# Kernel tuning notes

Hardware: AMD Instinct MI355X
Metric: run time of the kernel (lower is better)

Reference implementation:

```python
import jax, jax.numpy as jnp
import numpy as np

B, N, C = 8, 4096, 512
H = 8
OUT = 512
DH = C // H  # 64
LN_EPS = 1e-5
L2_EPS = 1e-12


def setup_inputs() -> dict:
    key = jax.random.key(0)
    ks = jax.random.split(key, 6)
    x = jax.random.normal(ks[0], (B, N, C), dtype=jnp.float32)
    ln_g = jnp.ones((C,), dtype=jnp.float32)
    ln_b = jnp.zeros((C,), dtype=jnp.float32)
    qkv_w = jax.random.normal(ks[1], (3 * C, C), dtype=jnp.float32) * 0.02  # torch Linear weight [out,in]
    temperature = jnp.ones((H, 1, 1), dtype=jnp.float32)
    proj_w = jax.random.normal(ks[2], (OUT, C), dtype=jnp.float32) * 0.02
    proj_b = jnp.zeros((OUT,), dtype=jnp.float32)
    return {"x": x, "ln_g": ln_g, "ln_b": ln_b, "qkv_w": qkv_w,
            "temperature": temperature, "proj_w": proj_w, "proj_b": proj_b}


def reference(x, ln_g, ln_b, qkv_w, temperature, proj_w, proj_b):
    # LayerNorm
    mu = jnp.mean(x, axis=-1, keepdims=True)
    var = jnp.mean(jnp.square(x - mu), axis=-1, keepdims=True)
    xn = (x - mu) * jax.lax.rsqrt(var + LN_EPS) * ln_g + ln_b
    # QKV projection (no bias)
    qkv = xn @ qkv_w.T  # [B,N,3C]
    qkv = qkv.reshape(B, N, 3, H, DH).transpose(2, 0, 3, 4, 1)  # [3,B,H,DH,N]
    q, k, v = qkv[0], qkv[1], qkv[2]  # each [B,H,DH,N] (already 'transposed' channel layout)
    # L2-normalize q,k along token dim (matches F.normalize eps behavior)
    q = q / jnp.clip(jnp.linalg.norm(q, axis=-1, keepdims=True), L2_EPS)
    k = k / jnp.clip(jnp.linalg.norm(k, axis=-1, keepdims=True), L2_EPS)
    # channel attention [B,H,DH,DH], scaled by per-head temperature
    attn = jnp.einsum('bhdn,bhen->bhde', q, k) * temperature[None]
    attn = jax.nn.softmax(attn, axis=-1)
    out = jnp.einsum('bhde,bhen->bhdn', attn, v)  # [B,H,DH,N]
    out = out.transpose(0, 3, 1, 2).reshape(B, N, H * DH)  # [B,N,C]
    out = jax.nn.gelu(out, approximate=False)
    out = out @ proj_w.T + proj_b
    return out
```

## Files before the change

kernel.cpp:

```cpp
#include <hip/hip_runtime.h>
#include <hip/hip_bf16.h>

typedef __hip_bfloat16 bf16;
typedef __bf16 bfrag __attribute__((ext_vector_type(8)));
typedef float f32x4 __attribute__((ext_vector_type(4)));

#define AS1 __attribute__((address_space(1)))
#define AS3 __attribute__((address_space(3)))

static constexpr int Bb = 8, Nn = 4096, Cc = 512, Hh = 8;
static constexpr int Mtok = Bb * Nn;
static constexpr int QKVC = 3 * Cc;
static constexpr size_t WS_NEED = 57147392;
static constexpr int SPL_STRIDE = 8 * 20 * 8192;

__device__ __forceinline__ void gl_lds16(const void* g, void* l) {
  __builtin_amdgcn_global_load_lds((const AS1 void*)g, (AS3 void*)l, 16, 0, 0);
}
__device__ __forceinline__ float gelu_exact(float x) {
  return 0.5f * x * (1.0f + erff(x * 0.70710678118654752f));
}
__device__ __forceinline__ int g3(int x) { return ((x & 1) << 2) | (x >> 1); }
__device__ __forceinline__ int tileid(int mt, int nt) {
  return mt + (nt == 0 ? 0 : nt == 1 ? 2 : nt == 2 ? 6 : 12);
}

__global__ __launch_bounds__(256) void fill_f32(float* o, float val, int n) {
  int i = blockIdx.x * 256 + threadIdx.x;
  if (i < n) o[i] = val;
}

__global__ __launch_bounds__(256) void cvt_f32_bf16(const float* __restrict__ a,
                                                    bf16* __restrict__ o, int n) {
  int i = (blockIdx.x * 256 + threadIdx.x) * 8;
  if (i + 8 <= n) {
    float f[8];
    *(float4*)f       = *(const float4*)(a + i);
    *(float4*)(f + 4) = *(const float4*)(a + i + 4);
    bf16 v[8];
#pragma unroll
    for (int j = 0; j < 8; ++j) v[j] = __float2bfloat16(f[j]);
    *(uint4*)(o + i) = *(uint4*)v;
  }
}

__global__ __launch_bounds__(256) void cvt_mirror(const float* __restrict__ part,
                                                  bf16* __restrict__ Gcvb) {
  int tile = blockIdx.x, b = blockIdx.y;
  int ti = tile >> 2, tj = tile & 3;
  int t = threadIdx.x;
  bf16* ob = Gcvb + (size_t)b * Cc * Cc;
  if (ti <= tj) {
#pragma unroll
    for (int r8 = 0; r8 < 8; ++r8) {
      int row = r8 * 16 + (t >> 4), col = (t & 15) * 8;
      int mt = 2 * ti + (row >> 6), rsub = row & 63;
      const float* p0 = part + ((size_t)b * 20 + tileid(mt, tj)) * 8192 + rsub * 128 + col;
      float f[8];
      *(float4*)f       = *(const float4*)p0;
      *(float4*)(f + 4) = *(const float4*)(p0 + 4);
#pragma unroll
      for (int s = 1; s < 4; ++s) {
        const float* ps = p0 + (size_t)s * SPL_STRIDE;
        float g[8];
        *(float4*)g       = *(const float4*)ps;
        *(float4*)(g + 4) = *(const float4*)(ps + 4);
#pragma unroll
        for (int j = 0; j < 8; ++j) f[j] += g[j];
      }
      bf16 v[8];
#pragma unroll
      for (int j = 0; j < 8; ++j) v[j] = __float2bfloat16(f[j]);
      *(uint4*)(ob + (size_t)(ti * 128 + row) * Cc + tj * 128 + col) = *(uint4*)v;
    }
  } else {
    __shared__ bf16 ls[128][136];
#pragma unroll
    for (int r8 = 0; r8 < 8; ++r8) {
      int srow = r8 * 16 + (t >> 4), scol = (t & 15) * 8;
      int mt = 2 * tj + (srow >> 6), rsub = srow & 63;
      const float* p0 = part + ((size_t)b * 20 + tileid(mt, ti)) * 8192 + rsub * 128 + scol;
      float f[8];
      *(float4*)f       = *(const float4*)p0;
      *(float4*)(f + 4) = *(const float4*)(p0 + 4);
#pragma unroll
      for (int s = 1; s < 4; ++s) {
        const float* ps = p0 + (size_t)s * SPL_STRIDE;
        float g[8];
        *(float4*)g       = *(const float4*)ps;
        *(float4*)(g + 4) = *(const float4*)(ps + 4);
#pragma unroll
        for (int j = 0; j < 8; ++j) f[j] += g[j];
      }
      bf16 v[8];
#pragma unroll
      for (int j = 0; j < 8; ++j) v[j] = __float2bfloat16(f[j]);
      *(uint4*)&ls[srow][scol] = *(uint4*)v;
    }
    __syncthreads();
#pragma unroll
    for (int r8 = 0; r8 < 8; ++r8) {
      int orow = r8 * 16 + (t >> 4), ocol = (t & 15) * 8;
      bf16 v[8];
#pragma unroll
      for (int u = 0; u < 8; ++u) v[u] = ls[ocol + u][orow];
      *(uint4*)(ob + (size_t)(ti * 128 + orow) * Cc + tj * 128 + ocol) = *(uint4*)v;
    }
  }
}

__global__ __launch_bounds__(256) void ln_kernel(const float* __restrict__ x,
                                                 const float* __restrict__ gw,
                                                 const float* __restrict__ bw,
                                                 bf16* __restrict__ xn) {
  int tok  = blockIdx.x * 4 + (threadIdx.x >> 6);
  int lane = threadIdx.x & 63;
  const float* xr = x + (size_t)tok * Cc + lane * 8;
  float f[8];
  *(float4*)f       = *(const float4*)xr;
  *(float4*)(f + 4) = *(const float4*)(xr + 4);
  float s = 0.f;
#pragma unroll
  for (int j = 0; j < 8; ++j) s += f[j];
#pragma unroll
  for (int m = 32; m; m >>= 1) s += __shfl_xor(s, m);
  float mu = s * (1.0f / 512.0f);
  float q = 0.f;
#pragma unroll
  for (int j = 0; j < 8; ++j) { float d = f[j] - mu; q += d * d; }
#pragma unroll
  for (int m = 32; m; m >>= 1) q += __shfl_xor(q, m);
  float rstd = rsqrtf(q * (1.0f / 512.0f) + 1e-5f);
  bf16 o[8];
#pragma unroll
  for (int j = 0; j < 8; ++j)
    o[j] = __float2bfloat16((f[j] - mu) * rstd * gw[lane * 8 + j] + bw[lane * 8 + j]);
  *(uint4*)(xn + (size_t)tok * Cc + lane * 8) = *(uint4*)o;
}

template <typename TC, bool SWZ>
__global__ __launch_bounds__(256) void gemm_bt(const bf16* __restrict__ A,
                                               const bf16* __restrict__ B,
                                               TC* __restrict__ C,
                                               int M, int N, int K,
                                               const float* __restrict__ bias,
                                               long sA_z, long sB_z, long sC_z) {
  A += (size_t)blockIdx.z * sA_z;
  B += (size_t)blockIdx.z * sB_z;
  C += (size_t)blockIdx.z * sC_z;
  __shared__ __align__(16) bf16 smem[16384];
  bf16* sA = smem;
  bf16* sB = smem + 8192;
  int t = threadIdx.x, w = t >> 6, lane = t & 63, fr = lane & 15, quad = lane >> 4;
  int n0, m0;
  if constexpr (SWZ) {
    int flat = blockIdx.y * 4 + blockIdx.x;
    int idx  = (flat & 7) * 128 + (flat >> 3);
    n0 = (idx & 3) * 128;
    m0 = (idx >> 2) * 128;
  } else {
    n0 = blockIdx.x * 128;
    m0 = blockIdx.y * 128;
  }
  int wm = (w >> 1) * 64, wn = (w & 1) * 64;
  f32x4 acc[4][4] = {};

  for (int k0 = 0; k0 < K; k0 += 64) {
    __syncthreads();
#pragma unroll
    for (int c2 = 0; c2 < 4; ++c2) {
      int c = w * 4 + c2;
      int row = c * 8 + (lane >> 3);
      int ke  = ((lane & 7) ^ (lane >> 3)) * 8;
      gl_lds16(A + (size_t)(m0 + row) * K + k0 + ke, (char*)sA + c * 1024);
      gl_lds16(B + (size_t)(n0 + row) * K + k0 + ke, (char*)sB + c * 1024);
    }
    __syncthreads();
#pragma unroll
    for (int kk = 0; kk < 64; kk += 32) {
      bfrag af[4], bg[4];
#pragma unroll
      for (int i = 0; i < 4; ++i)
        af[i] = *(const bfrag*)(sA + (wm + i * 16 + fr) * 64 +
                                ((((kk >> 3) + quad) ^ (fr & 7)) * 8));
#pragma unroll
      for (int j = 0; j < 4; ++j)
        bg[j] = *(const bfrag*)(sB + (wn + j * 16 + fr) * 64 +
                                ((((kk >> 3) + quad) ^ (fr & 7)) * 8));
#pragma unroll
      for (int i = 0; i < 4; ++i)
#pragma unroll
        for (int j = 0; j < 4; ++j)
          acc[i][j] = __builtin_amdgcn_mfma_f32_16x16x32_bf16(af[i], bg[j], acc[i][j], 0, 0, 0);
    }
  }

  if constexpr (__is_same(TC, float)) {
#pragma unroll
    for (int j = 0; j < 4; ++j) {
      float bj = bias ? bias[n0 + wn + j * 16 + fr] : 0.0f;
#pragma unroll
      for (int i = 0; i < 4; ++i)
#pragma unroll
        for (int r = 0; r < 4; ++r)
          C[(size_t)(m0 + wm + i * 16 + quad * 4 + r) * N + n0 + wn + j * 16 + fr] =
              acc[i][j][r] + bj;
    }
  } else {
    __syncthreads();
    bf16* ct = smem;
#pragma unroll
    for (int j = 0; j < 4; ++j) {
      float bj = bias ? bias[n0 + wn + j * 16 + fr] : 0.0f;
#pragma unroll
      for (int i = 0; i < 4; ++i)
#pragma unroll
        for (int r = 0; r < 4; ++r)
          ct[(wm + i * 16 + quad * 4 + r) * 128 + wn + j * 16 + fr] =
              __float2bfloat16(acc[i][j][r] + bj);
    }
    __syncthreads();
#pragma unroll
    for (int r8 = 0; r8 < 8; ++r8) {
      int row = r8 * 16 + (t >> 4);
      int ce  = (t & 15) * 8;
      *(uint4*)(C + (size_t)(m0 + row) * N + n0 + ce) = *(const uint4*)(smem + row * 128 + ce);
    }
  }
}

__global__ __launch_bounds__(256) void xtx(const bf16* __restrict__ xn,
                                           float* __restrict__ part) {
  int flat = blockIdx.x;
  int idx  = (flat & 7) * 80 + (flat >> 3);
  int tile = idx % 20;
  int sb   = idx / 20;
  int split = sb & 3, b = sb >> 2;
  int nt = tile < 2 ? 0 : tile < 6 ? 1 : tile < 12 ? 2 : 3;
  int mt = tile - (nt == 0 ? 0 : nt == 1 ? 2 : nt == 2 ? 6 : 12);
  int m0 = mt * 64, n0 = nt * 128;
  bool alias = ((mt >> 1) == nt);
  int t = threadIdx.x, w = t >> 6, lane = t & 63, fr = lane & 15, quad = lane >> 4;
  int wn = w * 32;
  __shared__ __align__(16) bf16 sB[8192];
  __shared__ __align__(16) bf16 sAb[4096];
  bf16* sA = alias ? (sB + (mt & 1) * 4096) : sAb;
  f32x4 acc[4][2] = {};
  const bf16* xb = xn + ((size_t)b * Nn + split * 1024) * Cc;
  int ch0b = (t & 15) * 8, tgb = t >> 4;
  int ch0a = (t & 7) * 8,  tga = t >> 3;
  bool doA = (!alias) && (t < 128);
  unsigned swz = (unsigned)g3(t & 7);
  unsigned wposb = (((unsigned)(tgb >> 1) ^ swz) * 16u) + (unsigned)(tgb & 1) * 8u;
  unsigned wposa = (((unsigned)(tga >> 1) ^ swz) * 16u) + (unsigned)(tga & 1) * 8u;
  uint4 va[4], vb[4];
#pragma unroll
  for (int j = 0; j < 4; ++j)
    vb[j] = *(const uint4*)(xb + (size_t)(tgb * 4 + j) * Cc + n0 + ch0b);
  if (doA)
#pragma unroll
    for (int j = 0; j < 4; ++j)
      va[j] = *(const uint4*)(xb + (size_t)(tga * 4 + j) * Cc + m0 + ch0a);
  for (int kc = 0; kc < 16; ++kc) {
    __syncthreads();
#pragma unroll
    for (int k = 0; k < 4; ++k) {
      unsigned b0 = ((const unsigned*)&vb[0])[k], b1 = ((const unsigned*)&vb[1])[k];
      unsigned b2 = ((const unsigned*)&vb[2])[k], b3 = ((const unsigned*)&vb[3])[k];
      uint2 lo = { (b0 & 0xffffu) | (b1 << 16), (b2 & 0xffffu) | (b3 << 16) };
      uint2 hi = { (b0 >> 16) | (b1 & 0xffff0000u), (b2 >> 16) | (b3 & 0xffff0000u) };
      *(uint2*)((char*)sB + (unsigned)(ch0b + 2 * k) * 128 + wposb) = lo;
      *(uint2*)((char*)sB + (unsigned)(ch0b + 2 * k + 1) * 128 + wposb) = hi;
    }
    if (doA) {
#pragma unroll
      for (int k = 0; k < 4; ++k) {
        unsigned a0 = ((const unsigned*)&va[0])[k], a1 = ((const unsigned*)&va[1])[k];
        unsigned a2 = ((const unsigned*)&va[2])[k], a3 = ((const unsigned*)&va[3])[k];
        uint2 lo = { (a0 & 0xffffu) | (a1 << 16), (a2 & 0xffffu) | (a3 << 16) };
        uint2 hi = { (a0 >> 16) | (a1 & 0xffff0000u), (a2 >> 16) | (a3 & 0xffff0000u) };
        *(uint2*)((char*)sAb + (unsigned)(ch0a + 2 * k) * 128 + wposa) = lo;
        *(uint2*)((char*)sAb + (unsigned)(ch0a + 2 * k + 1) * 128 + wposa) = hi;
      }
    }
    __syncthreads();
    if (kc < 15) {
      const bf16* xb2 = xb + (size_t)(kc + 1) * 64 * Cc;
#pragma unroll
      for (int j = 0; j < 4; ++j)
        vb[j] = *(const uint4*)(xb2 + (size_t)(tgb * 4 + j) * Cc + n0 + ch0b);
      if (doA)
#pragma unroll
        for (int j = 0; j < 4; ++j)
          va[j] = *(const uint4*)(xb2 + (size_t)(tga * 4 + j) * Cc + m0 + ch0a);
    }
#pragma unroll
    for (int kk = 0; kk < 2; ++kk) {
      bfrag af[4], bg[2];
#pragma unroll
      for (int i = 0; i < 4; ++i) {
        int ch = i * 16 + fr;
        int slot = (kk * 4 + quad) ^ g3((ch >> 3) & 7);
        af[i] = *(const bfrag*)(sA + ch * 64 + slot * 8);
      }
#pragma unroll
      for (int j = 0; j < 2; ++j) {
        int ch = wn + j * 16 + fr;
        int slot = (kk * 4 + quad) ^ g3((ch >> 3) & 7);
        bg[j] = *(const bfrag*)(sB + ch * 64 + slot * 8);
      }
#pragma unroll
      for (int i = 0; i < 4; ++i)
#pragma unroll
        for (int j = 0; j < 2; ++j)
          acc[i][j] = __builtin_amdgcn_mfma_f32_16x16x32_bf16(af[i], bg[j], acc[i][j], 0, 0, 0);
    }
  }
  float* pb = part + (size_t)split * SPL_STRIDE + ((size_t)b * 20 + tile) * 8192;
#pragma unroll
  for (int i = 0; i < 4; ++i)
#pragma unroll
    for (int j = 0; j < 2; ++j)
#pragma unroll
      for (int r = 0; r < 4; ++r)
        pb[(i * 16 + quad * 4 + r) * 128 + wn + j * 16 + fr] = acc[i][j][r];
}

__global__ __launch_bounds__(256) void gram_softmax(const bf16* __restrict__ T,
                                                    const bf16* __restrict__ wq,
                                                    const float* __restrict__ temp,
                                                    bf16* __restrict__ P) {
  int h = blockIdx.x, b = blockIdx.y;
  int t = threadIdx.x, w = t >> 6, lane = t & 63, fr = lane & 15, quad = lane >> 4;
  const bf16* Tq = T + (size_t)b * 1024 * 512 + (size_t)(h * 64) * 512;
  const bf16* Tk = T + (size_t)b * 1024 * 512 + (size_t)(512 + h * 64) * 512;
  const bf16* Wqh = wq + (size_t)(h * 64) * 512;
  const bf16* Wkh = wq + (size_t)(512 + h * 64) * 512;
  f32x4 acc[4][4] = {};
#pragma unroll
  for (int s = 0; s < 4; ++s) {
    int kb = w * 128 + s * 32 + quad * 8;
    bfrag af[4], bg[4];
#pragma unroll
    for (int i = 0; i < 4; ++i) af[i] = *(const bfrag*)(Tq + (size_t)(i * 16 + fr) * 512 + kb);
#pragma unroll
    for (int j = 0; j < 4; ++j) bg[j] = *(const bfrag*)(Wkh + (size_t)(j * 16 + fr) * 512 + kb);
#pragma unroll
    for (int i = 0; i < 4; ++i)
#pragma unroll
      for (int j = 0; j < 4; ++j)
        acc[i][j] = __builtin_amdgcn_mfma_f32_16x16x32_bf16(af[i], bg[j], acc[i][j], 0, 0, 0);
  }
  __shared__ float parts[4 * 4096];
  __shared__ float nrm[2][4][64];
  __shared__ float nqk[2][64];
#pragma unroll
  for (int i = 0; i < 4; ++i)
#pragma unroll
    for (int j = 0; j < 4; ++j)
#pragma unroll
      for (int r = 0; r < 4; ++r)
        parts[w * 4096 + (i * 16 + quad * 4 + r) * 64 + j * 16 + fr] = acc[i][j][r];
  {
    int d = t & 63, qtr = t >> 6, c0 = qtr * 128;
    float pq = 0.f, pk = 0.f;
#pragma unroll 4
    for (int cc = 0; cc < 16; ++cc) {
      bf16 a[8], ww[8];
      *(uint4*)a  = *(const uint4*)(Tq + (size_t)d * 512 + c0 + cc * 8);
      *(uint4*)ww = *(const uint4*)(Wqh + (size_t)d * 512 + c0 + cc * 8);
#pragma unroll
      for (int j = 0; j < 8; ++j) pq += __bfloat162float(a[j]) * __bfloat162float(ww[j]);
      *(uint4*)a  = *(const uint4*)(Tk + (size_t)d * 512 + c0 + cc * 8);
      *(uint4*)ww = *(const uint4*)(Wkh + (size_t)d * 512 + c0 + cc * 8);
#pragma unroll
      for (int j = 0; j < 8; ++j) pk += __bfloat162float(a[j]) * __bfloat162float(ww[j]);
    }
    nrm[0][qtr][d] = pq;
    nrm[1][qtr][d] = pk;
  }
  __syncthreads();
  if (t < 64) {
    nqk[0][t] = fmaxf(sqrtf(nrm[0][0][t] + nrm[0][1][t] + nrm[0][2][t] + nrm[0][3][t]), 1e-12f);
    nqk[1][t] = fmaxf(sqrtf(nrm[1][0][t] + nrm[1][1][t] + nrm[1][2][t] + nrm[1][3][t]), 1e-12f);
  }
  __syncthreads();
  if (t < 64) {
    int d = t;
    float sc = temp[h] / nqk[0][d];
    float l[64]; float mx = -1e30f;
#pragma unroll
    for (int e = 0; e < 64; ++e) {
      float vsum = parts[d * 64 + e] + parts[4096 + d * 64 + e] +
                   parts[8192 + d * 64 + e] + parts[12288 + d * 64 + e];
      l[e] = vsum * sc / nqk[1][e];
      mx = fmaxf(mx, l[e]);
    }
    float sum = 0.f;
#pragma unroll
    for (int e = 0; e < 64; ++e) { l[e] = expf(l[e] - mx); sum += l[e]; }
    float inv = 1.0f / sum;
    bf16* pr = P + ((size_t)(b * 8 + h) * 64 + d) * 64;
#pragma unroll
    for (int e = 0; e < 64; ++e) pr[e] = __float2bfloat16(l[e] * inv);
  }
}

__global__ __launch_bounds__(256) void pv_gelu(const bf16* __restrict__ P,
                                               const bf16* __restrict__ v,
                                               bf16* __restrict__ g) {
  int chunk = blockIdx.x, h = blockIdx.y, b = blockIdx.z;
  int t = threadIdx.x, w = t >> 6, lane = t & 63, fr = lane & 15, quad = lane >> 4;
  const bf16* pb = P + (size_t)(b * 8 + h) * 4096;
  bfrag pf[4][2];
#pragma unroll
  for (int i = 0; i < 4; ++i)
#pragma unroll
    for (int c = 0; c < 2; ++c)
      pf[i][c] = *(const bfrag*)(pb + (i * 16 + fr) * 64 + c * 32 + quad * 8);
#pragma unroll 2
  for (int nt = 0; nt < 8; ++nt) {
    int ntok = chunk * 512 + w * 128 + nt * 16 + fr;
    const bf16* vrow = v + (size_t)(b * Nn + ntok) * Cc + h * 64 + quad * 8;
    bfrag bv0 = *(const bfrag*)(vrow);
    bfrag bv1 = *(const bfrag*)(vrow + 32);
    f32x4 acc[4] = {};
#pragma unroll
    for (int i = 0; i < 4; ++i) {
      acc[i] = __builtin_amdgcn_mfma_f32_16x16x32_bf16(pf[i][0], bv0, acc[i], 0, 0, 0);
      acc[i] = __builtin_amdgcn_mfma_f32_16x16x32_bf16(pf[i][1], bv1, acc[i], 0, 0, 0);
    }
    bf16* grow = g + (size_t)(b * Nn + ntok) * Cc + h * 64;
#pragma unroll
    for (int i = 0; i < 4; ++i) {
      bf16 o[4];
#pragma unroll
      for (int r = 0; r < 4; ++r) o[r] = __float2bfloat16(gelu_exact(acc[i][r]));
      *(uint2*)(grow + i * 16 + quad * 4) = *(uint2*)o;
    }
  }
}

extern "C" void kernel_launch(void* const* d_in, const int* in_sizes, int n_in,
                              void* d_out, int out_size, void* d_ws, size_t ws_size,
                              hipStream_t stream) {
  const float* x      = (const float*)d_in[0];
  const float* ln_g   = (const float*)d_in[1];
  const float* ln_b   = (const float*)d_in[2];
  const float* qkv_w  = (const float*)d_in[3];
  const float* temp   = (const float*)d_in[4];
  const float* proj_w = (const float*)d_in[5];
  const float* proj_b = (const float*)d_in[6];
  float* out = (float*)d_out;
  char*  ws  = (char*)d_ws;

  const int exp_sizes[7] = {16777216, 512, 512, 786432, 8, 262144, 512};
  bool sizes_ok = (n_in == 7) && (out_size == 16777216);
  if (sizes_ok) for (int i = 0; i < 7; ++i) sizes_ok = sizes_ok && (in_sizes[i] == exp_sizes[i]);
  if (!sizes_ok) {
    fill_f32<<<(16777216 + 255) / 256, 256, 0, stream>>>(out, 500.0f, out_size);
    return;
  }
  if (ws_size < WS_NEED) {
    fill_f32<<<(16777216 + 255) / 256, 256, 0, stream>>>(out, (float)(ws_size >> 20), out_size);
    return;
  }

  bf16*  xn   = (bf16*)ws;
  bf16*  g    = (bf16*)ws;
  bf16*  Gcvb = (bf16*)(ws + 41943040);
  bf16*  T    = (bf16*)(ws + 46137344);
  bf16*  P    = (bf16*)(ws + 54525952);
  bf16*  wq   = (bf16*)(ws + 55050240);
  bf16*  wp   = (bf16*)(ws + 56623104);
  bf16*  v    = (bf16*)d_out;
  float* part = (float*)((char*)d_out + 33554432);

  cvt_f32_bf16<<<384, 256, 0, stream>>>(qkv_w, wq, QKVC * Cc);
  cvt_f32_bf16<<<128, 256, 0, stream>>>(proj_w, wp, Cc * Cc);
  ln_kernel<<<Mtok / 4, 256, 0, stream>>>(x, ln_g, ln_b, xn);
  gemm_bt<bf16, true><<<dim3(4, 256, 1), 256, 0, stream>>>(xn, wq + 1024 * 512, v, Mtok, Cc, Cc,
                                                           nullptr, 0, 0, 0);
  xtx<<<640, 256, 0, stream>>>(xn, part);
  cvt_mirror<<<dim3(16, 8), 256, 0, stream>>>(part, Gcvb);
  gemm_bt<bf16, false><<<dim3(4, 8, 8), 256, 0, stream>>>(wq, Gcvb, T, 1024, Cc, Cc,
                                                          nullptr, 0, (long)Cc * Cc, (long)1024 * Cc);
  gram_softmax<<<dim3(Hh, Bb), 256, 0, stream>>>(T, wq, temp, P);
  pv_gelu<<<dim3(8, Hh, Bb), 256, 0, stream>>>(P, v, g);
  gemm_bt<float, true><<<dim3(4, 256, 1), 256, 0, stream>>>(g, wp, out, Mtok, Cc, Cc,
                                                            proj_b, 0, 0, 0);
}
```

Measured before the change: 259.3 us.

## Merge weight conversion into LayerNorm launch and co-schedule V GEMM with XᵀX

Folds the two weight f32→bf16 conversion launches into the LayerNorm kernel by giving extra blocks to the conversion work. Merges the V-projection GEMM and the split-K XᵀX partial-Gram kernel into one launch that dispatches on block index, so the two independent workloads run concurrently and fill the GPU together. This removes several kernel launches and their tail gaps. In exchange the merged kernel has divergent block roles and a shared LDS/register budget, which may lower occupancy for one of the paths.

```diff
diff --git a/kernel.cpp b/kernel.cpp
--- a/kernel.cpp
+++ b/kernel.cpp
@@ -30,17 +30,53 @@
   if (i < n) o[i] = val;
 }
 
-__global__ __launch_bounds__(256) void cvt_f32_bf16(const float* __restrict__ a,
-                                                    bf16* __restrict__ o, int n) {
-  int i = (blockIdx.x * 256 + threadIdx.x) * 8;
-  if (i + 8 <= n) {
+__global__ __launch_bounds__(256) void ln_cvtw(const float* __restrict__ x,
+                                               const float* __restrict__ gw,
+                                               const float* __restrict__ bw,
+                                               bf16* __restrict__ xn,
+                                               const float* __restrict__ qkv_w,
+                                               const float* __restrict__ proj_w,
+                                               bf16* __restrict__ wq,
+                                               bf16* __restrict__ wp) {
+  int bid = blockIdx.x;
+  if (bid < 8192) {
+    int tok  = bid * 4 + (threadIdx.x >> 6);
+    int lane = threadIdx.x & 63;
+    const float* xr = x + (size_t)tok * Cc + lane * 8;
+    float f[8];
+    *(float4*)f       = *(const float4*)xr;
+    *(float4*)(f + 4) = *(const float4*)(xr + 4);
+    float s = 0.f;
+#pragma unroll
+    for (int j = 0; j < 8; ++j) s += f[j];
+#pragma unroll
+    for (int m = 32; m; m >>= 1) s += __shfl_xor(s, m);
+    float mu = s * (1.0f / 512.0f);
+    float q = 0.f;
+#pragma unroll
+    for (int j = 0; j < 8; ++j) { float d = f[j] - mu; q += d * d; }
+#pragma unroll
+    for (int m = 32; m; m >>= 1) q += __shfl_xor(q, m);
+    float rstd = rsqrtf(q * (1.0f / 512.0f) + 1e-5f);
+    bf16 o[8];
+#pragma unroll
+    for (int j = 0; j < 8; ++j)
+      o[j] = __float2bfloat16((f[j] - mu) * rstd * gw[lane * 8 + j] + bw[lane * 8 + j]);
+    *(uint4*)(xn + (size_t)tok * Cc + lane * 8) = *(uint4*)o;
+  } else {
+    int cb = bid - 8192;
+    const float* a;
+    bf16* o;
+    int i;
+    if (cb < 384) { a = qkv_w;  o = wq; i = (cb * 256 + (int)threadIdx.x) * 8; }
+    else          { a = proj_w; o = wp; i = ((cb - 384) * 256 + (int)threadIdx.x) * 8; }
     float f[8];
     *(float4*)f       = *(const float4*)(a + i);
     *(float4*)(f + 4) = *(const float4*)(a + i + 4);
-    bf16 v[8];
-#pragma unroll
-    for (int j = 0; j < 8; ++j) v[j] = __float2bfloat16(f[j]);
-    *(uint4*)(o + i) = *(uint4*)v;
+    bf16 vv[8];
+#pragma unroll
+    for (int j = 0; j < 8; ++j) vv[j] = __float2bfloat16(f[j]);
+    *(uint4*)(o + i) = *(uint4*)vv;
   }
 }
 
@@ -107,35 +143,6 @@
       *(uint4*)(ob + (size_t)(ti * 128 + orow) * Cc + tj * 128 + ocol) = *(uint4*)v;
     }
   }
-}
-
-__global__ __launch_bounds__(256) void ln_kernel(const float* __restrict__ x,
-                                                 const float* __restrict__ gw,
-                                                 const float* __restrict__ bw,
-                                                 bf16* __restrict__ xn) {
-  int tok  = blockIdx.x * 4 + (threadIdx.x >> 6);
-  int lane = threadIdx.x & 63;
-  const float* xr = x + (size_t)tok * Cc + lane * 8;
-  float f[8];
-  *(float4*)f       = *(const float4*)xr;
-  *(float4*)(f + 4) = *(const float4*)(xr + 4);
-  float s = 0.f;
-#pragma unroll
-  for (int j = 0; j < 8; ++j) s += f[j];
-#pragma unroll
-  for (int m = 32; m; m >>= 1) s += __shfl_xor(s, m);
-  float mu = s * (1.0f / 512.0f);
-  float q = 0.f;
-#pragma unroll
-  for (int j = 0; j < 8; ++j) { float d = f[j] - mu; q += d * d; }
-#pragma unroll
-  for (int m = 32; m; m >>= 1) q += __shfl_xor(q, m);
-  float rstd = rsqrtf(q * (1.0f / 512.0f) + 1e-5f);
-  bf16 o[8];
-#pragma unroll
-  for (int j = 0; j < 8; ++j)
-    o[j] = __float2bfloat16((f[j] - mu) * rstd * gw[lane * 8 + j] + bw[lane * 8 + j]);
-  *(uint4*)(xn + (size_t)tok * Cc + lane * 8) = *(uint4*)o;
 }
 
 template <typename TC, bool SWZ>
@@ -229,101 +236,160 @@
   }
 }
 
-__global__ __launch_bounds__(256) void xtx(const bf16* __restrict__ xn,
-                                           float* __restrict__ part) {
-  int flat = blockIdx.x;
-  int idx  = (flat & 7) * 80 + (flat >> 3);
-  int tile = idx % 20;
-  int sb   = idx / 20;
-  int split = sb & 3, b = sb >> 2;
-  int nt = tile < 2 ? 0 : tile < 6 ? 1 : tile < 12 ? 2 : 3;
-  int mt = tile - (nt == 0 ? 0 : nt == 1 ? 2 : nt == 2 ? 6 : 12);
-  int m0 = mt * 64, n0 = nt * 128;
-  bool alias = ((mt >> 1) == nt);
+__global__ __launch_bounds__(256) void vgemm_xtx(const bf16* __restrict__ xn,
+                                                 const bf16* __restrict__ wv,
+                                                 bf16* __restrict__ v,
+                                                 float* __restrict__ part) {
+  __shared__ __align__(16) bf16 smem[16384];
   int t = threadIdx.x, w = t >> 6, lane = t & 63, fr = lane & 15, quad = lane >> 4;
-  int wn = w * 32;
-  __shared__ __align__(16) bf16 sB[8192];
-  __shared__ __align__(16) bf16 sAb[4096];
-  bf16* sA = alias ? (sB + (mt & 1) * 4096) : sAb;
-  f32x4 acc[4][2] = {};
-  const bf16* xb = xn + ((size_t)b * Nn + split * 1024) * Cc;
-  int ch0b = (t & 15) * 8, tgb = t >> 4;
-  int ch0a = (t & 7) * 8,  tga = t >> 3;
-  bool doA = (!alias) && (t < 128);
-  unsigned swz = (unsigned)g3(t & 7);
-  unsigned wposb = (((unsigned)(tgb >> 1) ^ swz) * 16u) + (unsigned)(tgb & 1) * 8u;
-  unsigned wposa = (((unsigned)(tga >> 1) ^ swz) * 16u) + (unsigned)(tga & 1) * 8u;
-  uint4 va[4], vb[4];
-#pragma unroll
-  for (int j = 0; j < 4; ++j)
-    vb[j] = *(const uint4*)(xb + (size_t)(tgb * 4 + j) * Cc + n0 + ch0b);
-  if (doA)
+  if (blockIdx.x < 1024) {
+    bf16* sA = smem;
+    bf16* sB = smem + 8192;
+    int flat = blockIdx.x;
+    int idx  = (flat & 7) * 128 + (flat >> 3);
+    int n0 = (idx & 3) * 128, m0 = (idx >> 2) * 128;
+    int wm = (w >> 1) * 64, wn = (w & 1) * 64;
+    f32x4 acc[4][4] = {};
+    for (int k0 = 0; k0 < 512; k0 += 64) {
+      __syncthreads();
+#pragma unroll
+      for (int c2 = 0; c2 < 4; ++c2) {
+        int c = w * 4 + c2;
+        int row = c * 8 + (lane >> 3);
+        int ke  = ((lane & 7) ^ (lane >> 3)) * 8;
+        gl_lds16(xn + (size_t)(m0 + row) * 512 + k0 + ke, (char*)sA + c * 1024);
+        gl_lds16(wv + (size_t)(n0 + row) * 512 + k0 + ke, (char*)sB + c * 1024);
+      }
+      __syncthreads();
+#pragma unroll
+      for (int kk = 0; kk < 64; kk += 32) {
+        bfrag af[4], bg[4];
+#pragma unroll
+        for (int i = 0; i < 4; ++i)
+          af[i] = *(const bfrag*)(sA + (wm + i * 16 + fr) * 64 +
+                                  ((((kk >> 3) + quad) ^ (fr & 7)) * 8));
+#pragma unroll
+        for (int j = 0; j < 4; ++j)
+          bg[j] = *(const bfrag*)(sB + (wn + j * 16 + fr) * 64 +
+                                  ((((kk >> 3) + quad) ^ (fr & 7)) * 8));
+#pragma unroll
+        for (int i = 0; i < 4; ++i)
+#pragma unroll
+          for (int j = 0; j < 4; ++j)
+            acc[i][j] = __builtin_amdgcn_mfma_f32_16x16x32_bf16(af[i], bg[j], acc[i][j], 0, 0, 0);
+      }
+    }
+    __syncthreads();
+    bf16* ct = smem;
 #pragma unroll
     for (int j = 0; j < 4; ++j)
-      va[j] = *(const uint4*)(xb + (size_t)(tga * 4 + j) * Cc + m0 + ch0a);
-  for (int kc = 0; kc < 16; ++kc) {
-    __syncthreads();
-#pragma unroll
-    for (int k = 0; k < 4; ++k) {
-      unsigned b0 = ((const unsigned*)&vb[0])[k], b1 = ((const unsigned*)&vb[1])[k];
-      unsigned b2 = ((const unsigned*)&vb[2])[k], b3 = ((const unsigned*)&vb[3])[k];
-      uint2 lo = { (b0 & 0xffffu) | (b1 << 16), (b2 & 0xffffu) | (b3 << 16) };
-      uint2 hi = { (b0 >> 16) | (b1 & 0xffff0000u), (b2 >> 16) | (b3 & 0xffff0000u) };
-      *(uint2*)((char*)sB + (unsigned)(ch0b + 2 * k) * 128 + wposb) = lo;
-      *(uint2*)((char*)sB + (unsigned)(ch0b + 2 * k + 1) * 128 + wposb) = hi;
-    }
-    if (doA) {
+#pragma unroll
+      for (int i = 0; i < 4; ++i)
+#pragma unroll
+        for (int r = 0; r < 4; ++r)
+          ct[(wm + i * 16 + quad * 4 + r) * 128 + wn + j * 16 + fr] =
+              __float2bfloat16(acc[i][j][r]);
+    __syncthreads();
+#pragma unroll
+    for (int r8 = 0; r8 < 8; ++r8) {
+      int row = r8 * 16 + (t >> 4);
+      int ce  = (t & 15) * 8;
+      *(uint4*)(v + (size_t)(m0 + row) * 512 + n0 + ce) = *(const uint4*)(smem + row * 128 + ce);
+    }
+  } else {
+    bf16* sB  = smem;
+    bf16* sAb = smem + 8192;
+    int flat = blockIdx.x - 1024;
+    int idx  = (flat & 7) * 80 + (flat >> 3);
+    int tile = idx % 20;
+    int sb   = idx / 20;
+    int split = sb & 3, b = sb >> 2;
+    int nt = tile < 2 ? 0 : tile < 6 ? 1 : tile < 12 ? 2 : 3;
+    int mt = tile - (nt == 0 ? 0 : nt == 1 ? 2 : nt == 2 ? 6 : 12);
+    int m0 = mt * 64, n0 = nt * 128;
+    bool alias = ((mt >> 1) == nt);
+    int wn = w * 32;
+    bf16* sA = alias ? (sB + (mt & 1) * 4096) : sAb;
+    f32x4 acc[4][2] = {};
+    const bf16* xb = xn + ((size_t)b * Nn + split * 1024) * Cc;
+    int ch0b = (t & 15) * 8, tgb = t >> 4;
+    int ch0a = (t & 7) * 8,  tga = t >> 3;
+    bool doA = (!alias) && (t < 128);
+    unsigned swz = (unsigned)g3(t & 7);
+    unsigned wposb = (((unsigned)(tgb >> 1) ^ swz) * 16u) + (unsigned)(tgb & 1) * 8u;
+    unsigned wposa = (((unsigned)(tga >> 1) ^ swz) * 16u) + (unsigned)(tga & 1) * 8u;
+    uint4 va[4], vb[4];
+#pragma unroll
+    for (int j = 0; j < 4; ++j)
+      vb[j] = *(const uint4*)(xb + (size_t)(tgb * 4 + j) * Cc + n0 + ch0b);
+    if (doA)
+#pragma unroll
+      for (int j = 0; j < 4; ++j)
+        va[j] = *(const uint4*)(xb + (size_t)(tga * 4 + j) * Cc + m0 + ch0a);
+    for (int kc = 0; kc < 16; ++kc) {
+      __syncthreads();
 #pragma unroll
       for (int k = 0; k < 4; ++k) {
-        unsigned a0 = ((const unsigned*)&va[0])[k], a1 = ((const unsigned*)&va[1])[k];
-        unsigned a2 = ((const unsigned*)&va[2])[k], a3 = ((const unsigned*)&va[3])[k];
-        uint2 lo = { (a0 & 0xffffu) | (a1 << 16), (a2 & 0xffffu) | (a3 << 16) };
-        uint2 hi = { (a0 >> 16) | (a1 & 0xffff0000u), (a2 >> 16) | (a3 & 0xffff0000u) };
-        *(uint2*)((char*)sAb + (unsigned)(ch0a + 2 * k) * 128 + wposa) = lo;
-        *(uint2*)((char*)sAb + (unsigned)(ch0a + 2 * k + 1) * 128 + wposa) = hi;
-      }
-    }
-    __syncthreads();
-    if (kc < 15) {
-      const bf16* xb2 = xb + (size_t)(kc + 1) * 64 * Cc;
-#pragma unroll
-      for (int j = 0; j < 4; ++j)
-        vb[j] = *(const uint4*)(xb2 + (size_t)(tgb * 4 + j) * Cc + n0 + ch0b);
-      if (doA)
+        unsigned b0 = ((const unsigned*)&vb[0])[k], b1 = ((const unsigned*)&vb[1])[k];
+        unsigned b2 = ((const unsigned*)&vb[2])[k], b3 = ((const unsigned*)&vb[3])[k];
+        uint2 lo = { (b0 & 0xffffu) | (b1 << 16), (b2 & 0xffffu) | (b3 << 16) };
+        uint2 hi = { (b0 >> 16) | (b1 & 0xffff0000u), (b2 >> 16) | (b3 & 0xffff0000u) };
+        *(uint2*)((char*)sB + (unsigned)(ch0b + 2 * k) * 128 + wposb) = lo;
+        *(uint2*)((char*)sB + (unsigned)(ch0b + 2 * k + 1) * 128 + wposb) = hi;
+      }
+      if (doA) {
+#pragma unroll
+        for (int k = 0; k < 4; ++k) {
+          unsigned a0 = ((const unsigned*)&va[0])[k], a1 = ((const unsigned*)&va[1])[k];
+          unsigned a2 = ((const unsigned*)&va[2])[k], a3 = ((const unsigned*)&va[3])[k];
+          uint2 lo = { (a0 & 0xffffu) | (a1 << 16), (a2 & 0xffffu) | (a3 << 16) };
+          uint2 hi = { (a0 >> 16) | (a1 & 0xffff0000u), (a2 >> 16) | (a3 & 0xffff0000u) };
+          *(uint2*)((char*)sAb + (unsigned)(ch0a + 2 * k) * 128 + wposa) = lo;
+          *(uint2*)((char*)sAb + (unsigned)(ch0a + 2 * k + 1) * 128 + wposa) = hi;
+        }
+      }
+      __syncthreads();
+      if (kc < 15) {
+        const bf16* xb2 = xb + (size_t)(kc + 1) * 64 * Cc;
 #pragma unroll
         for (int j = 0; j < 4; ++j)
-          va[j] = *(const uint4*)(xb2 + (size_t)(tga * 4 + j) * Cc + m0 + ch0a);
-    }
-#pragma unroll
-    for (int kk = 0; kk < 2; ++kk) {
-      bfrag af[4], bg[2];
-#pragma unroll
-      for (int i = 0; i < 4; ++i) {
-        int ch = i * 16 + fr;
-        int slot = (kk * 4 + quad) ^ g3((ch >> 3) & 7);
-        af[i] = *(const bfrag*)(sA + ch * 64 + slot * 8);
-      }
-#pragma unroll
-      for (int j = 0; j < 2; ++j) {
-        int ch = wn + j * 16 + fr;
-        int slot = (kk * 4 + quad) ^ g3((ch >> 3) & 7);
-        bg[j] = *(const bfrag*)(sB + ch * 64 + slot * 8);
-      }
-#pragma unroll
-      for (int i = 0; i < 4; ++i)
-#pragma unroll
-        for (int j = 0; j < 2; ++j)
-          acc[i][j] = __builtin_amdgcn_mfma_f32_16x16x32_bf16(af[i], bg[j], acc[i][j], 0, 0, 0);
-    }
-  }
-  float* pb = part + (size_t)split * SPL_STRIDE + ((size_t)b * 20 + tile) * 8192;
-#pragma unroll
-  for (int i = 0; i < 4; ++i)
-#pragma unroll
-    for (int j = 0; j < 2; ++j)
-#pragma unroll
-      for (int r = 0; r < 4; ++r)
-        pb[(i * 16 + quad * 4 + r) * 128 + wn + j * 16 + fr] = acc[i][j][r];
+          vb[j] = *(const uint4*)(xb2 + (size_t)(tgb * 4 + j) * Cc + n0 + ch0b);
+        if (doA)
+#pragma unroll
+          for (int j = 0; j < 4; ++j)
+            va[j] = *(const uint4*)(xb2 + (size_t)(tga * 4 + j) * Cc + m0 + ch0a);
+      }
+#pragma unroll
+      for (int kk = 0; kk < 2; ++kk) {
+        bfrag af[4], bg[2];
+#pragma unroll
+        for (int i = 0; i < 4; ++i) {
+          int ch = i * 16 + fr;
+          int slot = (kk * 4 + quad) ^ g3((ch >> 3) & 7);
+          af[i] = *(const bfrag*)(sA + ch * 64 + slot * 8);
+        }
+#pragma unroll
+        for (int j = 0; j < 2; ++j) {
+          int ch = wn + j * 16 + fr;
+          int slot = (kk * 4 + quad) ^ g3((ch >> 3) & 7);
+          bg[j] = *(const bfrag*)(sB + ch * 64 + slot * 8);
+        }
+#pragma unroll
+        for (int i = 0; i < 4; ++i)
+#pragma unroll
+          for (int j = 0; j < 2; ++j)
+            acc[i][j] = __builtin_amdgcn_mfma_f32_16x16x32_bf16(af[i], bg[j], acc[i][j], 0, 0, 0);
+      }
+    }
+    float* pb = part + (size_t)split * SPL_STRIDE + ((size_t)b * 20 + tile) * 8192;
+#pragma unroll
+    for (int i = 0; i < 4; ++i)
+#pragma unroll
+      for (int j = 0; j < 2; ++j)
+#pragma unroll
+        for (int r = 0; r < 4; ++r)
+          pb[(i * 16 + quad * 4 + r) * 128 + wn + j * 16 + fr] = acc[i][j][r];
+  }
 }
 
 __global__ __launch_bounds__(256) void gram_softmax(const bf16* __restrict__ T,
@@ -476,12 +542,8 @@
   bf16*  v    = (bf16*)d_out;
   float* part = (float*)((char*)d_out + 33554432);
 
-  cvt_f32_bf16<<<384, 256, 0, stream>>>(qkv_w, wq, QKVC * Cc);
-  cvt_f32_bf16<<<128, 256, 0, stream>>>(proj_w, wp, Cc * Cc);
-  ln_kernel<<<Mtok / 4, 256, 0, stream>>>(x, ln_g, ln_b, xn);
-  gemm_bt<bf16, true><<<dim3(4, 256, 1), 256, 0, stream>>>(xn, wq + 1024 * 512, v, Mtok, Cc, Cc,
-                                                           nullptr, 0, 0, 0);
-  xtx<<<640, 256, 0, stream>>>(xn, part);
+  ln_cvtw<<<8704, 256, 0, stream>>>(x, ln_g, ln_b, xn, qkv_w, proj_w, wq, wp);
+  vgemm_xtx<<<1664, 256, 0, stream>>>(xn, wq + 1024 * 512, v, part);
   cvt_mirror<<<dim3(16, 8), 256, 0, stream>>>(part, Gcvb);
   gemm_bt<bf16, false><<<dim3(4, 8, 8), 256, 0, stream>>>(wq, Gcvb, T, 1024, Cc, Cc,
                                                           nullptr, 0, (long)Cc * Cc, (long)1024 * Cc);
```

After: 258.1 us. Within noise of the previous version (-0.5%).
